# Performance work log

Hardware: AMD Instinct MI355X
Metric: run time of the kernel (lower is better)

The kernel has to match this reference:

```python
import jax, jax.numpy as jnp
import numpy as np

N = 50000
E = 1_600_000
IN_C = 128
OUT_C = 128


def _glorot(key, shape):
    fan_in, fan_out = shape[0], shape[1]
    s = jnp.sqrt(6.0 / (fan_in + fan_out))
    return jax.random.uniform(key, shape, jnp.float32, -s, s)


def setup_inputs() -> dict:
    key = jax.random.key(0)
    ks = jax.random.split(key, 32)
    inp = {
        'X': jax.random.normal(ks[0], (N, IN_C), jnp.float32),
        'edge_index': jax.random.randint(ks[1], (2, E), 0, N, jnp.int64),
        'edge_weight': jax.random.uniform(ks[2], (E,), jnp.float32),
        'H': jax.random.normal(ks[3], (N, OUT_C), jnp.float32),
        'C': jax.random.normal(ks[4], (N, OUT_C), jnp.float32),
    }
    i = 5
    for g in ('i', 'f', 'c', 'o'):
        inp[f'Wx_{g}'] = _glorot(ks[i], (IN_C, OUT_C)); i += 1
        inp[f'bx_{g}'] = jnp.zeros((OUT_C,), jnp.float32)
        inp[f'Wh_{g}'] = _glorot(ks[i], (OUT_C, OUT_C)); i += 1
        inp[f'bh_{g}'] = jnp.zeros((OUT_C,), jnp.float32)
    for g in ('i', 'f', 'o'):
        inp[f'w_c_{g}'] = _glorot(ks[i], (1, OUT_C)); i += 1
    for g in ('i', 'f', 'c', 'o'):
        inp[f'b_{g}'] = jnp.zeros((1, OUT_C), jnp.float32)
    return inp


def reference(X, edge_index, edge_weight, H, C,
              Wx_i, bx_i, Wh_i, bh_i,
              Wx_f, bx_f, Wh_f, bh_f,
              Wx_c, bx_c, Wh_c, bh_c,
              Wx_o, bx_o, Wh_o, bh_o,
              w_c_i, w_c_f, w_c_o,
              b_i, b_f, b_c, b_o):
    n = X.shape[0]
    src, dst = edge_index[0], edge_index[1]
    # GCN normalization (add_self_loops=False): deg from destination (in-degree)
    deg = jax.ops.segment_sum(edge_weight, dst, num_segments=n)
    dis = jnp.where(deg > 0, jax.lax.rsqrt(jnp.where(deg > 0, deg, 1.0)), 0.0)
    norm = dis[src] * edge_weight * dis[dst]  # [E]

    def gcn(x, W, b):
        xw = x @ W                       # [n, OUT_C]
        msg = xw[src] * norm[:, None]    # gather + scale, [E, OUT_C]
        return jax.ops.segment_sum(msg, dst, num_segments=n) + b

    I = jax.nn.sigmoid(gcn(X, Wx_i, bx_i) + gcn(H, Wh_i, bh_i) + w_c_i * C + b_i)
    Fg = jax.nn.sigmoid(gcn(X, Wx_f, bx_f) + gcn(H, Wh_f, bh_f) + w_c_f * C + b_f)
    T = jnp.tanh(gcn(X, Wx_c, bx_c) + gcn(H, Wh_c, bh_c) + b_c)
    Cn = Fg * C + I * T
    O = jax.nn.sigmoid(gcn(X, Wx_o, bx_o) + gcn(H, Wh_o, bh_o) + w_c_o * Cn + b_o)
    Hn = O * jnp.tanh(Cn)
    return Hn, Cn
```

## Files before the change

### kernel.cpp

```cpp
#include <hip/hip_runtime.h>

__device__ __forceinline__ float bf2f(unsigned short u){
    union { unsigned int i; float f; } v; v.i = ((unsigned int)u) << 16; return v.f;
}
__device__ __forceinline__ unsigned short f2bf(float f){
    union { unsigned int i; float f; } v; v.f = f;
    unsigned int i = v.i;
    unsigned int r = i + 0x7FFFu + ((i >> 16) & 1u);
    return (unsigned short)(r >> 16);
}
__device__ __forceinline__ float sigm(float x){ return 1.0f / (1.0f + __expf(-x)); }

__device__ __forceinline__ float ldsel(const void* p, size_t idx, int fF){
    float r;
    if (fF) r = ((const float*)p)[idx];
    else    r = bf2f(((const unsigned short*)p)[idx]);
    return r;
}

typedef __attribute__((ext_vector_type(8))) short s8v;
typedef __attribute__((ext_vector_type(4))) float f4v;

__global__ void k_detect(const unsigned short* __restrict__ X,
                         const int* __restrict__ ei, int* __restrict__ flags){
    __shared__ int cnt, nz;
    if (threadIdx.x == 0){ cnt = 0; nz = 0; }
    __syncthreads();
    int ok = 0;
    for (int i = threadIdx.x; i < 2048; i += 256){
        int e = (X[i] >> 7) & 0xFF;
        if (e >= 96 && e <= 160) ok++;
    }
    atomicAdd(&cnt, ok);
    int nzl = 0;
    for (int i = threadIdx.x; i < 128; i += 256)
        if (ei[2*i + 1] != 0) nzl++;
    atomicAdd(&nz, nzl);
    __syncthreads();
    if (threadIdx.x == 0){
        flags[0] = (cnt < 1843) ? 1 : 0;
        flags[1] = (nz == 0)   ? 1 : 0;
    }
}

struct PackArgs {
    const void* Wx[4];
    const void* Wh[4];
    const void* bx[4];
    const void* bh[4];
};

__global__ void k_fused1(const void* __restrict__ X, const void* __restrict__ H,
                         unsigned int* __restrict__ XHb32,
                         const int* __restrict__ ei, int* __restrict__ cnt,
                         int* __restrict__ off,
                         PackArgs pa, unsigned short* __restrict__ Bp,
                         float* __restrict__ bias,
                         const int* __restrict__ flags,
                         int nbT, int nbC, int E, int N){
    int b = blockIdx.x;
    int fF = flags[0];
    if (b < nbT){
        int t = b*256 + threadIdx.x;
        if (t >= N * 64) return;
        int n = t >> 6, l = t & 63;
        unsigned int xw, hw;
        if (fF){
            float2 xv = ((const float2*)X)[(size_t)n*64 + l];
            float2 hv = ((const float2*)H)[(size_t)n*64 + l];
            xw = ((unsigned int)f2bf(xv.y) << 16) | f2bf(xv.x);
            hw = ((unsigned int)f2bf(hv.y) << 16) | f2bf(hv.x);
        } else {
            xw = ((const unsigned int*)X)[(size_t)n*64 + l];
            hw = ((const unsigned int*)H)[(size_t)n*64 + l];
        }
        XHb32[(size_t)n*128 + l]      = xw;
        XHb32[(size_t)n*128 + 64 + l] = hw;
    } else if (b < nbT + nbC){
        int e = (b - nbT)*256 + threadIdx.x;
        if (e >= E) return;
        int fI = flags[1];
        int d = fI ? ei[2*(size_t)E + 2*(size_t)e] : ei[(size_t)E + e];
        if ((unsigned)d >= (unsigned)N) return;
        off[e] = atomicAdd(&cnt[d], 1);
    } else {
        int t = (b - nbT - nbC)*256 + threadIdx.x;
        if (t < 4*8*8*64*8){
            int j    =  t        & 7;
            int lane = (t >> 3)  & 63;
            int kb   = (t >> 9)  & 7;
            int ct   = (t >> 12) & 7;
            int g    = (t >> 15) & 3;
            int k   = kb*32 + (lane >> 4)*8 + j;
            int col = ct*16 + (lane & 15);
            const void* p; size_t idx;
            if (k < 128){ p = pa.Wx[g]; idx = (size_t)k*128 + col; }
            else        { p = pa.Wh[g]; idx = (size_t)(k-128)*128 + col; }
            unsigned short v;
            if (fF) v = f2bf(((const float*)p)[idx]);
            else    v = ((const unsigned short*)p)[idx];
            Bp[t] = v;
        }
        if (t < 512){
            int g = t >> 7, c = t & 127;
            bias[t] = ldsel(pa.bx[g], c, fF) + ldsel(pa.bh[g], c, fF);
        }
    }
}

__global__ void k_scanA(const int* __restrict__ cnt, int* __restrict__ bsum, int n){
    __shared__ int sh[256];
    int t = threadIdx.x, i = blockIdx.x * 256 + t;
    sh[t] = (i < n) ? cnt[i] : 0;
    __syncthreads();
    for (int o = 128; o > 0; o >>= 1){
        if (t < o) sh[t] += sh[t + o];
        __syncthreads();
    }
    if (t == 0) bsum[blockIdx.x] = sh[0];
}
__global__ void k_scanB(const int* __restrict__ bsum, int* __restrict__ bsumoff, int nb){
    __shared__ int sh[256];
    int t = threadIdx.x;
    int v = (t < nb) ? bsum[t] : 0;
    sh[t] = v;
    __syncthreads();
    for (int o = 1; o < 256; o <<= 1){
        int u = (t >= o) ? sh[t - o] : 0;
        __syncthreads();
        sh[t] += u;
        __syncthreads();
    }
    bsumoff[t] = sh[t] - v;
}
__global__ void k_scanC(const int* __restrict__ cnt, const int* __restrict__ bsumoff,
                        int* __restrict__ rowstart, int n){
    __shared__ int sh[256];
    int t = threadIdx.x, i = blockIdx.x * 256 + t;
    int v = (i < n) ? cnt[i] : 0;
    sh[t] = v;
    __syncthreads();
    for (int o = 1; o < 256; o <<= 1){
        int u = (t >= o) ? sh[t - o] : 0;
        __syncthreads();
        sh[t] += u;
        __syncthreads();
    }
    int incl = sh[t];
    if (i < n)     rowstart[i] = bsumoff[blockIdx.x] + incl - v;
    if (i == n-1)  rowstart[n] = bsumoff[blockIdx.x] + incl;
}

__global__ void k_scatter(const int* __restrict__ ei, const void* __restrict__ ew,
                          const int* __restrict__ rowstart, const int* __restrict__ off,
                          int2* __restrict__ recs, const int* __restrict__ flags,
                          int E, int N){
    int e = blockIdx.x * 256 + threadIdx.x;
    if (e >= E) return;
    int fF = flags[0], fI = flags[1];
    int s, d;
    if (fI){ s = ei[2*(size_t)e]; d = ei[2*(size_t)E + 2*(size_t)e]; }
    else   { s = ei[e];           d = ei[(size_t)E + e]; }
    if ((unsigned)d >= (unsigned)N) return;
    float w = 0.f; int ss = 0;
    if ((unsigned)s < (unsigned)N){ w = ldsel(ew, e, fF); ss = s; }
    int2 r; r.x = ss; r.y = __float_as_int(w);
    recs[rowstart[d] + off[e]] = r;
}

__global__ __launch_bounds__(256)
void k_degdis(const int2* __restrict__ recs, const int* __restrict__ rowstart,
              float* __restrict__ dis, int N){
    int gw = (blockIdx.x * 256 + threadIdx.x) >> 6;
    int lane = threadIdx.x & 63;
    if (gw >= N) return;
    int beg = rowstart[gw], end = rowstart[gw + 1];
    float sw = 0.f;
    for (int i = beg + lane; i < end; i += 64) sw += __int_as_float(recs[i].y);
    for (int o = 32; o > 0; o >>= 1) sw += __shfl_down(sw, o);
    if (lane == 0) dis[gw] = (sw > 0.f) ? rsqrtf(sw) : 0.f;
}

__global__ __launch_bounds__(256)
void k_gather(const int2* __restrict__ recs, const int* __restrict__ rowstart,
              const float* __restrict__ dis, const uint4* __restrict__ XHb128,
              uint4* __restrict__ AXH128, int N){
    int node = (blockIdx.x * 256 + threadIdx.x) >> 6;
    int lane = threadIdx.x & 63;
    if (node >= N) return;
    int half = lane >> 5;
    int sub  = lane & 31;
    int beg = rowstart[node], end = rowstart[node + 1];
    float disd = dis[node];
    float a0=0.f,a1=0.f,a2=0.f,a3=0.f,a4=0.f,a5=0.f,a6=0.f,a7=0.f;

#define ACC8(v, n)                                              \
    a0 += (n) * bf2f((unsigned short)((v).x & 0xffff));         \
    a1 += (n) * bf2f((unsigned short)((v).x >> 16));            \
    a2 += (n) * bf2f((unsigned short)((v).y & 0xffff));         \
    a3 += (n) * bf2f((unsigned short)((v).y >> 16));            \
    a4 += (n) * bf2f((unsigned short)((v).z & 0xffff));         \
    a5 += (n) * bf2f((unsigned short)((v).z >> 16));            \
    a6 += (n) * bf2f((unsigned short)((v).w & 0xffff));         \
    a7 += (n) * bf2f((unsigned short)((v).w >> 16));

    int i = beg;
    for (; i + 3 < end; i += 4){
        int2 rA = recs[i + half];
        int2 rB = recs[i + 2 + half];
        uint4 vA = XHb128[(size_t)rA.x*32 + sub];
        uint4 vB = XHb128[(size_t)rB.x*32 + sub];
        float nA = dis[rA.x] * __int_as_float(rA.y) * disd;
        float nB = dis[rB.x] * __int_as_float(rB.y) * disd;
        ACC8(vA, nA);
        ACC8(vB, nB);
    }
    if (end - i >= 2){
        int2 rA = recs[i + half];
        uint4 vA = XHb128[(size_t)rA.x*32 + sub];
        float nA = dis[rA.x] * __int_as_float(rA.y) * disd;
        ACC8(vA, nA);
        i += 2;
    }
    if (i < end){
        int2 rA = recs[i];
        uint4 vA = XHb128[(size_t)rA.x*32 + sub];
        float nA = (half == 0) ? dis[rA.x] * __int_as_float(rA.y) * disd : 0.f;
        ACC8(vA, nA);
    }
#undef ACC8

    a0 += __shfl_xor(a0, 32, 64);
    a1 += __shfl_xor(a1, 32, 64);
    a2 += __shfl_xor(a2, 32, 64);
    a3 += __shfl_xor(a3, 32, 64);
    a4 += __shfl_xor(a4, 32, 64);
    a5 += __shfl_xor(a5, 32, 64);
    a6 += __shfl_xor(a6, 32, 64);
    a7 += __shfl_xor(a7, 32, 64);

    if (half == 0){
        uint4 o;
        o.x = ((unsigned int)f2bf(a1) << 16) | f2bf(a0);
        o.y = ((unsigned int)f2bf(a3) << 16) | f2bf(a2);
        o.z = ((unsigned int)f2bf(a5) << 16) | f2bf(a4);
        o.w = ((unsigned int)f2bf(a7) << 16) | f2bf(a6);
        AXH128[(size_t)node*32 + sub] = o;
    }
}

struct EpiArgs {
    const void *C, *wci, *wcf, *wco, *bi, *bff, *bc, *bo;
};

__global__ __launch_bounds__(256)
void k_gemm(const unsigned short* __restrict__ AXH,
            const unsigned short* __restrict__ Bp, const float* __restrict__ bias,
            EpiArgs ea, void* __restrict__ outp, const int* __restrict__ flags, int N){
    int tid  = threadIdx.x;
    int w    = tid >> 6, lane = tid & 63;
    int node0 = blockIdx.x * 32;
    int fF = flags[0];

    f4v acc[2][8];
#pragma unroll
    for (int m = 0; m < 2; m++)
#pragma unroll
        for (int c = 0; c < 8; c++) acc[m][c] = (f4v){0.f,0.f,0.f,0.f};

    const unsigned short* a0base = AXH + (size_t)(node0 + (lane & 15))*256 + (lane >> 4)*8;
    const unsigned short* a1base = a0base + 16*256;
#pragma unroll
    for (int kb = 0; kb < 8; kb++){
        s8v af0 = *(const s8v*)(a0base + kb*32);
        s8v af1 = *(const s8v*)(a1base + kb*32);
#pragma unroll
        for (int ct8 = 0; ct8 < 8; ct8++){
            int g = ct8 >> 1, sub = ct8 & 1;
            const s8v bfrag = *(const s8v*)(Bp + g*32768 + (size_t)(w*2 + sub)*4096
                                            + kb*512 + lane*8);
            acc[0][ct8] = __builtin_amdgcn_mfma_f32_16x16x32_bf16(af0, bfrag, acc[0][ct8], 0, 0, 0);
            acc[1][ct8] = __builtin_amdgcn_mfma_f32_16x16x32_bf16(af1, bfrag, acc[1][ct8], 0, 0, 0);
        }
    }

    int q = lane >> 4, cl = lane & 15;
#pragma unroll
    for (int sub = 0; sub < 2; sub++){
        int c = w*32 + sub*16 + cl;
        float bvi = bias[0*128 + c], bvf = bias[1*128 + c];
        float bvc = bias[2*128 + c], bvo = bias[3*128 + c];
        float wci = ldsel(ea.wci, c, fF), wcf = ldsel(ea.wcf, c, fF), wco = ldsel(ea.wco, c, fF);
        float bi  = ldsel(ea.bi, c, fF),  bff = ldsel(ea.bff, c, fF);
        float bc  = ldsel(ea.bc, c, fF),  bo  = ldsel(ea.bo, c, fF);
#pragma unroll
        for (int m = 0; m < 2; m++){
#pragma unroll
            for (int r = 0; r < 4; r++){
                int node = node0 + m*16 + q*4 + r;
                if (node >= N) continue;
                size_t gidx = (size_t)node*128 + c;
                float Cv = ldsel(ea.C, gidx, fF);
                float pi  = acc[m][0+sub][r] + bvi;
                float pf  = acc[m][2+sub][r] + bvf;
                float pcv = acc[m][4+sub][r] + bvc;
                float po  = acc[m][6+sub][r] + bvo;
                float Iv = sigm(pi + wci*Cv + bi);
                float Fv = sigm(pf + wcf*Cv + bff);
                float Tv = tanhf(pcv + bc);
                float Cn = Fv*Cv + Iv*Tv;
                float Ov = sigm(po + wco*Cn + bo);
                float Hn = Ov * tanhf(Cn);
                if (fF){
                    ((float*)outp)[gidx] = Hn;
                    ((float*)outp)[(size_t)N*128 + gidx] = Cn;
                } else {
                    ((unsigned short*)outp)[gidx] = f2bf(Hn);
                    ((unsigned short*)outp)[(size_t)N*128 + gidx] = f2bf(Cn);
                }
            }
        }
    }
}

extern "C" void kernel_launch(void* const* d_in, const int* in_sizes, int n_in,
                              void* d_out, int out_size, void* d_ws, size_t ws_size,
                              hipStream_t stream){
    const void* X  = d_in[0];
    const int*  ei = (const int*)d_in[1];
    const void* ew = d_in[2];
    const void* H  = d_in[3];
    const void* C  = d_in[4];
    const int N = in_sizes[0] / 128;
    const int E = in_sizes[2];

    char* ws = (char*)d_ws;
    int*   cnt          = (int*)  (ws);
    float* dis          = (float*)(ws + ((size_t)256 << 10));
    int*   rowstart     = (int*)  (ws + ((size_t)512 << 10));
    int*   bsum         = (int*)  (ws + ((size_t)768 << 10));
    int*   bsumoff      = (int*)  (ws + ((size_t)772 << 10));
    int*   flags        = (int*)  (ws + ((size_t)776 << 10));
    unsigned short* Bp  = (unsigned short*)(ws + ((size_t)1 << 20));
    float* bias         = (float*)(ws + ((size_t)1 << 20) + ((size_t)256 << 10));
    int*   off          = (int*)  (ws + ((size_t)2 << 20));
    unsigned int* AXH32 = (unsigned int*)(ws + ((size_t)2 << 20));
    int2*  recs         = (int2*) (ws + ((size_t)28 << 20));
    unsigned int* XHb32 = (unsigned int*)(ws + ((size_t)41 << 20));

    hipMemsetAsync(cnt, 0, (size_t)256 << 10, stream);
    k_detect<<<1, 256, 0, stream>>>((const unsigned short*)X, ei, flags);

    PackArgs pa;
    pa.Wx[0]=d_in[5];  pa.bx[0]=d_in[6];  pa.Wh[0]=d_in[7];  pa.bh[0]=d_in[8];
    pa.Wx[1]=d_in[9];  pa.bx[1]=d_in[10]; pa.Wh[1]=d_in[11]; pa.bh[1]=d_in[12];
    pa.Wx[2]=d_in[13]; pa.bx[2]=d_in[14]; pa.Wh[2]=d_in[15]; pa.bh[2]=d_in[16];
    pa.Wx[3]=d_in[17]; pa.bx[3]=d_in[18]; pa.Wh[3]=d_in[19]; pa.bh[3]=d_in[20];

    int nbT = (N*64 + 255)/256;
    int nbC = (E + 255)/256;
    k_fused1<<<nbT + nbC + 512, 256, 0, stream>>>(X, H, XHb32, ei, cnt, off,
                                                  pa, Bp, bias, flags, nbT, nbC, E, N);

    int nbA = (N + 255)/256;
    k_scanA<<<nbA, 256, 0, stream>>>(cnt, bsum, N);
    k_scanB<<<1, 256, 0, stream>>>(bsum, bsumoff, nbA);
    k_scanC<<<nbA, 256, 0, stream>>>(cnt, bsumoff, rowstart, N);

    k_scatter<<<(E + 255)/256, 256, 0, stream>>>(ei, ew, rowstart, off, recs, flags, E, N);
    k_degdis<<<(N*64 + 255)/256, 256, 0, stream>>>(recs, rowstart, dis, N);
    k_gather<<<(N*64 + 255)/256, 256, 0, stream>>>(recs, rowstart, dis,
                                                   (const uint4*)XHb32,
                                                   (uint4*)AXH32, N);

    EpiArgs ea;
    ea.C   = C;
    ea.wci = d_in[21];
    ea.wcf = d_in[22];
    ea.wco = d_in[23];
    ea.bi  = d_in[24];
    ea.bff = d_in[25];
    ea.bc  = d_in[26];
    ea.bo  = d_in[27];
    k_gemm<<<(N + 31)/32, 256, 0, stream>>>((const unsigned short*)AXH32, Bp, bias,
                                            ea, d_out, flags, N);
}
```

Before: 501.4 us.

## Split fused prep kernel into count, bf16 convert and pack kernels; widen per-thread work

```diff
diff --git a/kernel.cpp b/kernel.cpp
--- a/kernel.cpp
+++ b/kernel.cpp
@@ -50,61 +50,68 @@
     const void* bh[4];
 };
 
-__global__ void k_fused1(const void* __restrict__ X, const void* __restrict__ H,
-                         unsigned int* __restrict__ XHb32,
-                         const int* __restrict__ ei, int* __restrict__ cnt,
-                         int* __restrict__ off,
-                         PackArgs pa, unsigned short* __restrict__ Bp,
-                         float* __restrict__ bias,
-                         const int* __restrict__ flags,
-                         int nbT, int nbC, int E, int N){
-    int b = blockIdx.x;
+__global__ void k_tobf(const void* __restrict__ X, const void* __restrict__ H,
+                       uint4* __restrict__ XHb128, const int* __restrict__ flags,
+                       int N){
+    int t = blockIdx.x*256 + threadIdx.x;
+    if (t >= N*32) return;
+    int n = t >> 5, i = t & 31;
     int fF = flags[0];
-    if (b < nbT){
-        int t = b*256 + threadIdx.x;
-        if (t >= N * 64) return;
-        int n = t >> 6, l = t & 63;
-        unsigned int xw, hw;
-        if (fF){
-            float2 xv = ((const float2*)X)[(size_t)n*64 + l];
-            float2 hv = ((const float2*)H)[(size_t)n*64 + l];
-            xw = ((unsigned int)f2bf(xv.y) << 16) | f2bf(xv.x);
-            hw = ((unsigned int)f2bf(hv.y) << 16) | f2bf(hv.x);
-        } else {
-            xw = ((const unsigned int*)X)[(size_t)n*64 + l];
-            hw = ((const unsigned int*)H)[(size_t)n*64 + l];
-        }
-        XHb32[(size_t)n*128 + l]      = xw;
-        XHb32[(size_t)n*128 + 64 + l] = hw;
-    } else if (b < nbT + nbC){
-        int e = (b - nbT)*256 + threadIdx.x;
-        if (e >= E) return;
-        int fI = flags[1];
+    int q = (i < 16) ? i : i - 16;
+    uint4 o;
+    if (fF){
+        const float4* src = (const float4*)((i < 16) ? X : H);
+        float4 a = src[(size_t)n*32 + q*2];
+        float4 b = src[(size_t)n*32 + q*2 + 1];
+        o.x = ((unsigned int)f2bf(a.y) << 16) | f2bf(a.x);
+        o.y = ((unsigned int)f2bf(a.w) << 16) | f2bf(a.z);
+        o.z = ((unsigned int)f2bf(b.y) << 16) | f2bf(b.x);
+        o.w = ((unsigned int)f2bf(b.w) << 16) | f2bf(b.z);
+    } else {
+        const uint4* src = (const uint4*)((i < 16) ? X : H);
+        o = src[(size_t)n*16 + q];
+    }
+    XHb128[(size_t)n*32 + i] = o;
+}
+
+__global__ void k_cnt(const int* __restrict__ ei, int* __restrict__ cnt,
+                      int* __restrict__ off, const int* __restrict__ flags,
+                      int E, int N){
+    int base = blockIdx.x*1024 + threadIdx.x;
+    int fI = flags[1];
+#pragma unroll
+    for (int k = 0; k < 4; k++){
+        int e = base + k*256;
+        if (e >= E) break;
         int d = fI ? ei[2*(size_t)E + 2*(size_t)e] : ei[(size_t)E + e];
-        if ((unsigned)d >= (unsigned)N) return;
+        if ((unsigned)d >= (unsigned)N) continue;
         off[e] = atomicAdd(&cnt[d], 1);
-    } else {
-        int t = (b - nbT - nbC)*256 + threadIdx.x;
-        if (t < 4*8*8*64*8){
-            int j    =  t        & 7;
-            int lane = (t >> 3)  & 63;
-            int kb   = (t >> 9)  & 7;
-            int ct   = (t >> 12) & 7;
-            int g    = (t >> 15) & 3;
-            int k   = kb*32 + (lane >> 4)*8 + j;
-            int col = ct*16 + (lane & 15);
-            const void* p; size_t idx;
-            if (k < 128){ p = pa.Wx[g]; idx = (size_t)k*128 + col; }
-            else        { p = pa.Wh[g]; idx = (size_t)(k-128)*128 + col; }
-            unsigned short v;
-            if (fF) v = f2bf(((const float*)p)[idx]);
-            else    v = ((const unsigned short*)p)[idx];
-            Bp[t] = v;
-        }
-        if (t < 512){
-            int g = t >> 7, c = t & 127;
-            bias[t] = ldsel(pa.bx[g], c, fF) + ldsel(pa.bh[g], c, fF);
-        }
+    }
+}
+
+__global__ void k_pack(PackArgs pa, unsigned short* __restrict__ Bp,
+                       float* __restrict__ bias, const int* __restrict__ flags){
+    int t = blockIdx.x*256 + threadIdx.x;
+    int fF = flags[0];
+    {
+        int j    =  t        & 7;
+        int lane = (t >> 3)  & 63;
+        int kb   = (t >> 9)  & 7;
+        int ct   = (t >> 12) & 7;
+        int g    = (t >> 15) & 3;
+        int k   = kb*32 + (lane >> 4)*8 + j;
+        int col = ct*16 + (lane & 15);
+        const void* p; size_t idx;
+        if (k < 128){ p = pa.Wx[g]; idx = (size_t)k*128 + col; }
+        else        { p = pa.Wh[g]; idx = (size_t)(k-128)*128 + col; }
+        unsigned short v;
+        if (fF) v = f2bf(((const float*)p)[idx]);
+        else    v = ((const unsigned short*)p)[idx];
+        Bp[t] = v;
+    }
+    if (t < 512){
+        int g = t >> 7, c = t & 127;
+        bias[t] = ldsel(pa.bx[g], c, fF) + ldsel(pa.bh[g], c, fF);
     }
 }
 
@@ -155,17 +162,21 @@
                           const int* __restrict__ rowstart, const int* __restrict__ off,
                           int2* __restrict__ recs, const int* __restrict__ flags,
                           int E, int N){
-    int e = blockIdx.x * 256 + threadIdx.x;
-    if (e >= E) return;
+    int base = blockIdx.x*512 + threadIdx.x;
     int fF = flags[0], fI = flags[1];
-    int s, d;
-    if (fI){ s = ei[2*(size_t)e]; d = ei[2*(size_t)E + 2*(size_t)e]; }
-    else   { s = ei[e];           d = ei[(size_t)E + e]; }
-    if ((unsigned)d >= (unsigned)N) return;
-    float w = 0.f; int ss = 0;
-    if ((unsigned)s < (unsigned)N){ w = ldsel(ew, e, fF); ss = s; }
-    int2 r; r.x = ss; r.y = __float_as_int(w);
-    recs[rowstart[d] + off[e]] = r;
+#pragma unroll
+    for (int k = 0; k < 2; k++){
+        int e = base + k*256;
+        if (e >= E) break;
+        int s, d;
+        if (fI){ s = ei[2*(size_t)e]; d = ei[2*(size_t)E + 2*(size_t)e]; }
+        else   { s = ei[e];           d = ei[(size_t)E + e]; }
+        if ((unsigned)d >= (unsigned)N) continue;
+        float w = 0.f; int ss = 0;
+        if ((unsigned)s < (unsigned)N){ w = ldsel(ew, e, fF); ss = s; }
+        int2 r; r.x = ss; r.y = __float_as_int(w);
+        recs[rowstart[d] + off[e]] = r;
+    }
 }
 
 __global__ __launch_bounds__(256)
@@ -357,17 +368,16 @@
     pa.Wx[2]=d_in[13]; pa.bx[2]=d_in[14]; pa.Wh[2]=d_in[15]; pa.bh[2]=d_in[16];
     pa.Wx[3]=d_in[17]; pa.bx[3]=d_in[18]; pa.Wh[3]=d_in[19]; pa.bh[3]=d_in[20];
 
-    int nbT = (N*64 + 255)/256;
-    int nbC = (E + 255)/256;
-    k_fused1<<<nbT + nbC + 512, 256, 0, stream>>>(X, H, XHb32, ei, cnt, off,
-                                                  pa, Bp, bias, flags, nbT, nbC, E, N);
+    k_cnt<<<(E + 1023)/1024, 256, 0, stream>>>(ei, cnt, off, flags, E, N);
+    k_tobf<<<(N*32 + 255)/256, 256, 0, stream>>>(X, H, (uint4*)XHb32, flags, N);
+    k_pack<<<512, 256, 0, stream>>>(pa, Bp, bias, flags);
 
     int nbA = (N + 255)/256;
     k_scanA<<<nbA, 256, 0, stream>>>(cnt, bsum, N);
     k_scanB<<<1, 256, 0, stream>>>(bsum, bsumoff, nbA);
     k_scanC<<<nbA, 256, 0, stream>>>(cnt, bsumoff, rowstart, N);
 
-    k_scatter<<<(E + 255)/256, 256, 0, stream>>>(ei, ew, rowstart, off, recs, flags, E, N);
+    k_scatter<<<(E + 511)/512, 256, 0, stream>>>(ei, ew, rowstart, off, recs, flags, E, N);
     k_degdis<<<(N*64 + 255)/256, 256, 0, stream>>>(recs, rowstart, dis, N);
     k_gather<<<(N*64 + 255)/256, 256, 0, stream>>>(recs, rowstart, dis,
                                                    (const uint4*)XHb32,
```

Measured after the change: 506.2 us. No clear change (+1.0%).
